# Performance work log

Measured on AMD Instinct MI355X. Metric: run time of the kernel, lower is better.

Reference implementation:

```python
import jax, jax.numpy as jnp
import numpy as np

TAU = 0.5  # matches init_kwargs tau
EPS = 1e-8  # torch CosineSimilarity eps


def setup_inputs() -> dict:
    key = jax.random.key(0)
    k1, k2 = jax.random.split(key)
    B, D = 4096, 256
    return {
        "z_orig": jax.random.normal(k1, (B, D), dtype=jnp.float32),
        "z_augment": jax.random.normal(k2, (B, D), dtype=jnp.float32),
    }


def reference(z_orig, z_augment):
    B = z_orig.shape[0]
    N = 2 * B
    # collect_z = cat([z_augment, z_orig])  -> [2B, D]
    z = jnp.concatenate([z_augment, z_orig], axis=0)
    # cosine similarity matrix via L2 normalize + matmul
    zn = z / jnp.maximum(jnp.linalg.norm(z, axis=-1, keepdims=True), EPS)
    S = zn @ zn.T  # [2B, 2B]
    # positives: diag offsets +B and -B
    pos = jnp.concatenate([jnp.diagonal(S, B), jnp.diagonal(S, -B)])[:, None]  # [2B, 1]
    # negatives: everything except main diag and the +/-B diagonals.
    # Static indices (shape-dependent only), computed in numpy at trace time.
    mask = ~((np.eye(N, k=B) + np.eye(N, k=-B) + np.eye(N)).astype(bool))
    flat_idx = jnp.asarray(np.nonzero(mask.reshape(-1))[0])  # [2B*(2B-2)]
    neg = S.reshape(-1)[flat_idx].reshape(N, N - 2)  # row-major order matches torch boolean mask
    logits = jnp.concatenate([pos, neg], axis=1) / TAU  # [2B, 2B-1]
    # CrossEntropy with label 0 for every row, reduction='sum', then / 2B
    loss = -jax.nn.log_softmax(logits, axis=-1)[:, 0]
    return jnp.sum(loss) / N
```

## Files before the change

kernel.cpp:

```cpp
#include <hip/hip_runtime.h>
#include <hip/hip_bf16.h>

typedef __attribute__((ext_vector_type(8))) short bf16x8;
typedef __attribute__((ext_vector_type(4))) float f32x4;

#define N_ROWS 8192
#define B_HALF 4096
#define D_DIM 256
#define NUT   2080
#define EXP2C 2.885390081777927f

#define WS_ZN       0
#define WS_ROWACC   4194304
#define WS_POS      4227072
#define WS_DIAG     4259840
#define WS_ACC      4292608
#define WS_CNT      4292612

__device__ __forceinline__ unsigned short f2bf(float f) {
    __hip_bfloat16 h = __float2bfloat16(f);
    union { __hip_bfloat16 h; unsigned short u; } c; c.h = h; return c.u;
}

__device__ __forceinline__ float fexp2(float x) { return exp2f(x); }

__device__ __forceinline__ void async_copy16(const void* g, void* l) {
    __builtin_amdgcn_global_load_lds(
        (const __attribute__((address_space(1))) unsigned int*)g,
        (__attribute__((address_space(3))) unsigned int*)l,
        16, 0, 0);
}

__global__ __launch_bounds__(256) void normalize_k(
    const float* __restrict__ z_orig, const float* __restrict__ z_aug,
    unsigned short* __restrict__ zn, float* __restrict__ rowAcc,
    float* __restrict__ accum, unsigned int* __restrict__ cnt)
{
    if (blockIdx.x == 0 && threadIdx.x == 0) { *accum = 0.0f; *cnt = 0u; }
    const int row  = blockIdx.x * 4 + (threadIdx.x >> 6);
    const int lane = threadIdx.x & 63;
    if (lane == 0) rowAcc[row] = 0.0f;
    const float* src = (row < B_HALF) ? (z_aug  + (size_t)row * D_DIM)
                                      : (z_orig + (size_t)(row - B_HALF) * D_DIM);
    float4 v = ((const float4*)src)[lane];
    float ss = v.x*v.x + v.y*v.y + v.z*v.z + v.w*v.w;
    #pragma unroll
    for (int m = 1; m < 64; m <<= 1) ss += __shfl_xor(ss, m);
    float inv = 1.0f / fmaxf(sqrtf(ss), 1e-8f);
    ushort4 o;
    o.x = f2bf(v.x * inv); o.y = f2bf(v.y * inv);
    o.z = f2bf(v.z * inv); o.w = f2bf(v.w * inv);
    ((ushort4*)(zn + (size_t)row * D_DIM))[lane] = o;
}

__global__ __launch_bounds__(256, 3) void tile_k(
    const unsigned short* __restrict__ zn,
    float* __restrict__ rowAcc,
    float* __restrict__ posv,
    float* __restrict__ diagE)
{
    __shared__ unsigned short As[128 * 64];
    __shared__ unsigned short Bs[128 * 64];

    const int bid = blockIdx.x;
    int rb = (int)((129.0f - sqrtf(16641.0f - 8.0f * (float)bid)) * 0.5f);
    rb = rb < 0 ? 0 : (rb > 63 ? 63 : rb);
    while ((rb + 1) * (129 - (rb + 1)) / 2 <= bid) ++rb;
    while (rb * (129 - rb) / 2 > bid) --rb;
    const int cb = rb + (bid - rb * (129 - rb) / 2);

    const int t    = threadIdx.x;
    const int rowBase = rb * 128;
    const int colBase = cb * 128;
    const int lane   = t & 63;
    const int w      = t >> 6;
    const int wy     = w >> 1;
    const int wx     = w & 1;
    const int lane15 = lane & 15;
    const int quad   = lane >> 4;

    f32x4 acc[4][4];
    #pragma unroll
    for (int i = 0; i < 4; ++i)
        #pragma unroll
        for (int j = 0; j < 4; ++j)
            acc[i][j] = (f32x4){0.f, 0.f, 0.f, 0.f};

    const char* zA = (const char*)zn + (size_t)rowBase * 512;
    const char* zB = (const char*)zn + (size_t)colBase * 512;

    const int rloc = t >> 3;
    const int q16  = ((t & 7) ^ (rloc & 7)) * 16;
    const int rA = wy * 64 + lane15;
    const int rB = wx * 64 + lane15;
    const int sw = lane15 & 7;

    #pragma unroll 1
    for (int kk = 0; kk < 4; ++kk) {
        const int koff = kk * 128;
        #pragma unroll
        for (int s = 0; s < 4; ++s) {
            const size_t goff = (size_t)(s * 32 + rloc) * 512 + koff + q16;
            async_copy16(zA + goff, (char*)As + s * 4096 + w * 1024);
            async_copy16(zB + goff, (char*)Bs + s * 4096 + w * 1024);
        }
        __syncthreads();

        #pragma unroll
        for (int kk2 = 0; kk2 < 2; ++kk2) {
            const int pa = (((kk2 * 4 + quad) ^ sw) << 4);
            bf16x8 a[4], b[4];
            #pragma unroll
            for (int mi = 0; mi < 4; ++mi)
                a[mi] = *(const bf16x8*)((const char*)As + (rA + mi * 16) * 128 + pa);
            #pragma unroll
            for (int ni = 0; ni < 4; ++ni)
                b[ni] = *(const bf16x8*)((const char*)Bs + (rB + ni * 16) * 128 + pa);
            #pragma unroll
            for (int mi = 0; mi < 4; ++mi)
                #pragma unroll
                for (int ni = 0; ni < 4; ++ni)
                    acc[mi][ni] = __builtin_amdgcn_mfma_f32_16x16x32_bf16(
                                      a[mi], b[ni], acc[mi][ni], 0, 0, 0);
        }
        __syncthreads();
    }

    const bool diagLane = (wy == wx) && ((lane15 >> 2) == quad);
    const int  rsel = lane15 & 3;
    if (cb == rb && diagLane) {
        #pragma unroll
        for (int mi = 0; mi < 4; ++mi) {
            int grow = rowBase + wy * 64 + mi * 16 + lane15;
            diagE[grow] = fexp2(acc[mi][mi][rsel] * EXP2C);
        }
    }
    if (cb == rb + 32 && diagLane) {
        #pragma unroll
        for (int mi = 0; mi < 4; ++mi) {
            int grow = rowBase + wy * 64 + mi * 16 + lane15;
            float v = acc[mi][mi][rsel];
            posv[grow] = v;
            posv[grow + B_HALF] = v;
        }
    }

    #pragma unroll
    for (int mi = 0; mi < 4; ++mi)
        #pragma unroll
        for (int ni = 0; ni < 4; ++ni)
            #pragma unroll
            for (int r = 0; r < 4; ++r)
                acc[mi][ni][r] = fexp2(acc[mi][ni][r] * EXP2C);

    #pragma unroll
    for (int mi = 0; mi < 4; ++mi)
        #pragma unroll
        for (int r = 0; r < 4; ++r) {
            float s = acc[mi][0][r] + acc[mi][1][r] + acc[mi][2][r] + acc[mi][3][r];
            s += __shfl_xor(s, 1);
            s += __shfl_xor(s, 2);
            s += __shfl_xor(s, 4);
            s += __shfl_xor(s, 8);
            if (lane15 == 0)
                atomicAdd(&rowAcc[rowBase + wy * 64 + mi * 16 + quad * 4 + r], s);
        }

    if (cb != rb) {
        #pragma unroll
        for (int ni = 0; ni < 4; ++ni) {
            float s = 0.0f;
            #pragma unroll
            for (int mi = 0; mi < 4; ++mi)
                s += acc[mi][ni][0] + acc[mi][ni][1] + acc[mi][ni][2] + acc[mi][ni][3];
            s += __shfl_xor(s, 16);
            s += __shfl_xor(s, 32);
            if (quad == 0)
                atomicAdd(&rowAcc[colBase + wx * 64 + ni * 16 + lane15], s);
        }
    }
}

__global__ __launch_bounds__(256) void loss_k(
    const float* __restrict__ rowAcc, const float* __restrict__ posv,
    const float* __restrict__ diagE, float* __restrict__ accum,
    unsigned int* __restrict__ cnt, float* __restrict__ out)
{
    const int i = blockIdx.x * 256 + threadIdx.x;
    float s = rowAcc[i] - diagE[i];
    float loss = __logf(s) - 2.0f * posv[i];

    #pragma unroll
    for (int m = 1; m < 64; m <<= 1) loss += __shfl_xor(loss, m);
    __shared__ float red[4];
    if ((threadIdx.x & 63) == 0) red[threadIdx.x >> 6] = loss;
    __syncthreads();
    if (threadIdx.x == 0) {
        float bs = red[0] + red[1] + red[2] + red[3];
        atomicAdd(accum, bs);
        __threadfence();
        unsigned int old = atomicAdd(cnt, 1u);
        if (old == 31u) {
            __threadfence();
            float total = atomicAdd(accum, 0.0f);
            out[0] = total * (1.0f / (float)N_ROWS);
        }
    }
}

extern "C" void kernel_launch(void* const* d_in, const int* in_sizes, int n_in,
                              void* d_out, int out_size, void* d_ws, size_t ws_size,
                              hipStream_t stream) {
    const float* z_orig = (const float*)d_in[0];
    const float* z_aug  = (const float*)d_in[1];
    char* ws = (char*)d_ws;
    unsigned short* zn  = (unsigned short*)(ws + WS_ZN);
    float* rowAcc       = (float*)(ws + WS_ROWACC);
    float* posv         = (float*)(ws + WS_POS);
    float* diagE        = (float*)(ws + WS_DIAG);
    float* accum        = (float*)(ws + WS_ACC);
    unsigned int* cnt   = (unsigned int*)(ws + WS_CNT);

    normalize_k<<<N_ROWS / 4, 256, 0, stream>>>(z_orig, z_aug, zn, rowAcc, accum, cnt);
    tile_k<<<NUT, 256, 0, stream>>>(zn, rowAcc, posv, diagE);
    loss_k<<<N_ROWS / 256, 256, 0, stream>>>(rowAcc, posv, diagE, accum, cnt,
                                             (float*)d_out);
}
```

Before: 103.7 us.

## Switch similarity GEMM to FP8 MFMA with full-K LDS tiles and row-block reuse

Normalized rows are now stored as FP8 (e4m3) rather than bf16, and the tile kernel uses the fp8 16x16x32 MFMA, which halves operand bytes and doubles MFMA throughput per instruction. Each block keeps its whole 128x256 A row tile resident in LDS and walks up to four column tiles, prefetching the next B tile while the current one's exp/reduction epilogue runs. Grid indexing changes from a triangular bid decode to a 2D grid with early exit. The cost is reduced precision of the cosine similarities, which are then exponentiated, plus 64KB of LDS per block that limits occupancy.

```diff
diff --git a/kernel.cpp b/kernel.cpp
--- a/kernel.cpp
+++ b/kernel.cpp
@@ -1,28 +1,26 @@
 #include <hip/hip_runtime.h>
 #include <hip/hip_bf16.h>
 
-typedef __attribute__((ext_vector_type(8))) short bf16x8;
 typedef __attribute__((ext_vector_type(4))) float f32x4;
 
 #define N_ROWS 8192
 #define B_HALF 4096
-#define D_DIM 256
-#define NUT   2080
 #define EXP2C 2.885390081777927f
 
 #define WS_ZN       0
-#define WS_ROWACC   4194304
-#define WS_POS      4227072
-#define WS_DIAG     4259840
-#define WS_ACC      4292608
-#define WS_CNT      4292612
-
-__device__ __forceinline__ unsigned short f2bf(float f) {
-    __hip_bfloat16 h = __float2bfloat16(f);
-    union { __hip_bfloat16 h; unsigned short u; } c; c.h = h; return c.u;
-}
-
-__device__ __forceinline__ float fexp2(float x) { return exp2f(x); }
+#define WS_ROWACC   2097152
+#define WS_POS      2129920
+#define WS_DIAG     2162688
+#define WS_ACC      2195456
+#define WS_CNT      2195460
+
+__device__ __forceinline__ float fexp2(float x) {
+#if __has_builtin(__builtin_amdgcn_exp2f)
+    return __builtin_amdgcn_exp2f(x);
+#else
+    return exp2f(x);
+#endif
+}
 
 __device__ __forceinline__ void async_copy16(const void* g, void* l) {
     __builtin_amdgcn_global_load_lds(
@@ -33,150 +31,161 @@
 
 __global__ __launch_bounds__(256) void normalize_k(
     const float* __restrict__ z_orig, const float* __restrict__ z_aug,
-    unsigned short* __restrict__ zn, float* __restrict__ rowAcc,
+    unsigned char* __restrict__ zn, float* __restrict__ rowAcc,
     float* __restrict__ accum, unsigned int* __restrict__ cnt)
 {
     if (blockIdx.x == 0 && threadIdx.x == 0) { *accum = 0.0f; *cnt = 0u; }
     const int row  = blockIdx.x * 4 + (threadIdx.x >> 6);
     const int lane = threadIdx.x & 63;
     if (lane == 0) rowAcc[row] = 0.0f;
-    const float* src = (row < B_HALF) ? (z_aug  + (size_t)row * D_DIM)
-                                      : (z_orig + (size_t)(row - B_HALF) * D_DIM);
+    const float* src = (row < B_HALF) ? (z_aug  + (size_t)row * 256)
+                                      : (z_orig + (size_t)(row - B_HALF) * 256);
     float4 v = ((const float4*)src)[lane];
     float ss = v.x*v.x + v.y*v.y + v.z*v.z + v.w*v.w;
     #pragma unroll
     for (int m = 1; m < 64; m <<= 1) ss += __shfl_xor(ss, m);
     float inv = 1.0f / fmaxf(sqrtf(ss), 1e-8f);
-    ushort4 o;
-    o.x = f2bf(v.x * inv); o.y = f2bf(v.y * inv);
-    o.z = f2bf(v.z * inv); o.w = f2bf(v.w * inv);
-    ((ushort4*)(zn + (size_t)row * D_DIM))[lane] = o;
-}
-
-__global__ __launch_bounds__(256, 3) void tile_k(
-    const unsigned short* __restrict__ zn,
+    int pk = 0;
+    pk = __builtin_amdgcn_cvt_pk_fp8_f32(v.x * inv, v.y * inv, pk, false);
+    pk = __builtin_amdgcn_cvt_pk_fp8_f32(v.z * inv, v.w * inv, pk, true);
+    ((int*)(zn + (size_t)row * 256))[lane] = pk;
+}
+
+__global__ __launch_bounds__(256) void tile_k(
+    const unsigned char* __restrict__ zn,
     float* __restrict__ rowAcc,
     float* __restrict__ posv,
     float* __restrict__ diagE)
 {
-    __shared__ unsigned short As[128 * 64];
-    __shared__ unsigned short Bs[128 * 64];
-
-    const int bid = blockIdx.x;
-    int rb = (int)((129.0f - sqrtf(16641.0f - 8.0f * (float)bid)) * 0.5f);
-    rb = rb < 0 ? 0 : (rb > 63 ? 63 : rb);
-    while ((rb + 1) * (129 - (rb + 1)) / 2 <= bid) ++rb;
-    while (rb * (129 - rb) / 2 > bid) --rb;
-    const int cb = rb + (bid - rb * (129 - rb) / 2);
-
-    const int t    = threadIdx.x;
-    const int rowBase = rb * 128;
-    const int colBase = cb * 128;
+    __shared__ unsigned char As[128 * 256];
+    __shared__ unsigned char Bs[128 * 256];
+
+    const int rb  = blockIdx.y;
+    const int cb0 = rb + blockIdx.x * 4;
+    if (cb0 > 63) return;
+    const int nc  = min(4, 64 - cb0);
+
+    const int t      = threadIdx.x;
     const int lane   = t & 63;
     const int w      = t >> 6;
     const int wy     = w >> 1;
     const int wx     = w & 1;
     const int lane15 = lane & 15;
     const int quad   = lane >> 4;
-
-    f32x4 acc[4][4];
+    const int rowBase = rb * 128;
+
+    const int rloc = t >> 4;
+    const int q16  = ((t & 15) ^ rloc) * 16;
+    const int ldsW = w * 1024;
+
+    const unsigned char* gA = zn + (size_t)rowBase * 256;
     #pragma unroll
-    for (int i = 0; i < 4; ++i)
-        #pragma unroll
-        for (int j = 0; j < 4; ++j)
-            acc[i][j] = (f32x4){0.f, 0.f, 0.f, 0.f};
-
-    const char* zA = (const char*)zn + (size_t)rowBase * 512;
-    const char* zB = (const char*)zn + (size_t)colBase * 512;
-
-    const int rloc = t >> 3;
-    const int q16  = ((t & 7) ^ (rloc & 7)) * 16;
-    const int rA = wy * 64 + lane15;
-    const int rB = wx * 64 + lane15;
-    const int sw = lane15 & 7;
-
-    #pragma unroll 1
-    for (int kk = 0; kk < 4; ++kk) {
-        const int koff = kk * 128;
-        #pragma unroll
-        for (int s = 0; s < 4; ++s) {
-            const size_t goff = (size_t)(s * 32 + rloc) * 512 + koff + q16;
-            async_copy16(zA + goff, (char*)As + s * 4096 + w * 1024);
-            async_copy16(zB + goff, (char*)Bs + s * 4096 + w * 1024);
-        }
+    for (int s = 0; s < 8; ++s)
+        async_copy16(gA + (size_t)(s * 16 + rloc) * 256 + q16, As + s * 4096 + ldsW);
+    if (cb0 != rb) {
+        const unsigned char* gB = zn + (size_t)cb0 * 128 * 256;
+        #pragma unroll
+        for (int s = 0; s < 8; ++s)
+            async_copy16(gB + (size_t)(s * 16 + rloc) * 256 + q16, Bs + s * 4096 + ldsW);
+    }
+
+    const int rA = (wy * 64 + lane15) * 256;
+    const int rB = (wx * 64 + lane15) * 256;
+
+    for (int j = 0; j < nc; ++j) {
+        const int cb = cb0 + j;
+        const unsigned char* Bbase = (cb == rb) ? As : Bs;
+
         __syncthreads();
 
-        #pragma unroll
-        for (int kk2 = 0; kk2 < 2; ++kk2) {
-            const int pa = (((kk2 * 4 + quad) ^ sw) << 4);
-            bf16x8 a[4], b[4];
+        f32x4 acc[4][4];
+        #pragma unroll
+        for (int i = 0; i < 4; ++i)
+            #pragma unroll
+            for (int jj = 0; jj < 4; ++jj)
+                acc[i][jj] = (f32x4){0.f, 0.f, 0.f, 0.f};
+
+        #pragma unroll
+        for (int ks = 0; ks < 8; ++ks) {
+            const int sa = (((2 * ks + (quad >> 1)) ^ lane15) << 4) | ((quad & 1) << 3);
+            long a[4], b[4];
             #pragma unroll
             for (int mi = 0; mi < 4; ++mi)
-                a[mi] = *(const bf16x8*)((const char*)As + (rA + mi * 16) * 128 + pa);
+                a[mi] = *(const long*)(As + rA + mi * 4096 + sa);
             #pragma unroll
             for (int ni = 0; ni < 4; ++ni)
-                b[ni] = *(const bf16x8*)((const char*)Bs + (rB + ni * 16) * 128 + pa);
+                b[ni] = *(const long*)(Bbase + rB + ni * 4096 + sa);
             #pragma unroll
             for (int mi = 0; mi < 4; ++mi)
                 #pragma unroll
                 for (int ni = 0; ni < 4; ++ni)
-                    acc[mi][ni] = __builtin_amdgcn_mfma_f32_16x16x32_bf16(
+                    acc[mi][ni] = __builtin_amdgcn_mfma_f32_16x16x32_fp8_fp8(
                                       a[mi], b[ni], acc[mi][ni], 0, 0, 0);
         }
+
         __syncthreads();
-    }
-
-    const bool diagLane = (wy == wx) && ((lane15 >> 2) == quad);
-    const int  rsel = lane15 & 3;
-    if (cb == rb && diagLane) {
-        #pragma unroll
-        for (int mi = 0; mi < 4; ++mi) {
-            int grow = rowBase + wy * 64 + mi * 16 + lane15;
-            diagE[grow] = fexp2(acc[mi][mi][rsel] * EXP2C);
-        }
-    }
-    if (cb == rb + 32 && diagLane) {
-        #pragma unroll
-        for (int mi = 0; mi < 4; ++mi) {
-            int grow = rowBase + wy * 64 + mi * 16 + lane15;
-            float v = acc[mi][mi][rsel];
-            posv[grow] = v;
-            posv[grow + B_HALF] = v;
-        }
-    }
-
-    #pragma unroll
-    for (int mi = 0; mi < 4; ++mi)
-        #pragma unroll
-        for (int ni = 0; ni < 4; ++ni)
-            #pragma unroll
-            for (int r = 0; r < 4; ++r)
-                acc[mi][ni][r] = fexp2(acc[mi][ni][r] * EXP2C);
-
-    #pragma unroll
-    for (int mi = 0; mi < 4; ++mi)
-        #pragma unroll
-        for (int r = 0; r < 4; ++r) {
-            float s = acc[mi][0][r] + acc[mi][1][r] + acc[mi][2][r] + acc[mi][3][r];
-            s += __shfl_xor(s, 1);
-            s += __shfl_xor(s, 2);
-            s += __shfl_xor(s, 4);
-            s += __shfl_xor(s, 8);
-            if (lane15 == 0)
-                atomicAdd(&rowAcc[rowBase + wy * 64 + mi * 16 + quad * 4 + r], s);
-        }
-
-    if (cb != rb) {
-        #pragma unroll
-        for (int ni = 0; ni < 4; ++ni) {
-            float s = 0.0f;
-            #pragma unroll
-            for (int mi = 0; mi < 4; ++mi)
-                s += acc[mi][ni][0] + acc[mi][ni][1] + acc[mi][ni][2] + acc[mi][ni][3];
-            s += __shfl_xor(s, 16);
-            s += __shfl_xor(s, 32);
-            if (quad == 0)
-                atomicAdd(&rowAcc[colBase + wx * 64 + ni * 16 + lane15], s);
+
+        if (j + 1 < nc) {
+            const unsigned char* gB = zn + (size_t)(cb + 1) * 128 * 256;
+            #pragma unroll
+            for (int s = 0; s < 8; ++s)
+                async_copy16(gB + (size_t)(s * 16 + rloc) * 256 + q16,
+                             Bs + s * 4096 + ldsW);
+        }
+
+        const int colBase = cb * 128;
+        const bool diagLane = (wy == wx) && ((lane15 >> 2) == quad);
+        const int  rsel = lane15 & 3;
+        if (cb == rb && diagLane) {
+            #pragma unroll
+            for (int mi = 0; mi < 4; ++mi) {
+                int grow = rowBase + wy * 64 + mi * 16 + lane15;
+                diagE[grow] = fexp2(acc[mi][mi][rsel] * EXP2C);
+            }
+        }
+        if (cb == rb + 32 && diagLane) {
+            #pragma unroll
+            for (int mi = 0; mi < 4; ++mi) {
+                int grow = rowBase + wy * 64 + mi * 16 + lane15;
+                float v = acc[mi][mi][rsel];
+                posv[grow] = v;
+                posv[grow + B_HALF] = v;
+            }
+        }
+
+        #pragma unroll
+        for (int mi = 0; mi < 4; ++mi)
+            #pragma unroll
+            for (int ni = 0; ni < 4; ++ni)
+                #pragma unroll
+                for (int r = 0; r < 4; ++r)
+                    acc[mi][ni][r] = fexp2(acc[mi][ni][r] * EXP2C);
+
+        #pragma unroll
+        for (int mi = 0; mi < 4; ++mi)
+            #pragma unroll
+            for (int r = 0; r < 4; ++r) {
+                float s = acc[mi][0][r] + acc[mi][1][r] + acc[mi][2][r] + acc[mi][3][r];
+                s += __shfl_xor(s, 1);
+                s += __shfl_xor(s, 2);
+                s += __shfl_xor(s, 4);
+                s += __shfl_xor(s, 8);
+                if (lane15 == 0)
+                    atomicAdd(&rowAcc[rowBase + wy * 64 + mi * 16 + quad * 4 + r], s);
+            }
+
+        if (cb != rb) {
+            #pragma unroll
+            for (int ni = 0; ni < 4; ++ni) {
+                float s = 0.0f;
+                #pragma unroll
+                for (int mi = 0; mi < 4; ++mi)
+                    s += acc[mi][ni][0] + acc[mi][ni][1] + acc[mi][ni][2] + acc[mi][ni][3];
+                s += __shfl_xor(s, 16);
+                s += __shfl_xor(s, 32);
+                if (quad == 0)
+                    atomicAdd(&rowAcc[colBase + wx * 64 + ni * 16 + lane15], s);
+            }
         }
     }
 }
@@ -214,7 +223,7 @@
     const float* z_orig = (const float*)d_in[0];
     const float* z_aug  = (const float*)d_in[1];
     char* ws = (char*)d_ws;
-    unsigned short* zn  = (unsigned short*)(ws + WS_ZN);
+    unsigned char* zn   = (unsigned char*)(ws + WS_ZN);
     float* rowAcc       = (float*)(ws + WS_ROWACC);
     float* posv         = (float*)(ws + WS_POS);
     float* diagE        = (float*)(ws + WS_DIAG);
@@ -222,7 +231,7 @@
     unsigned int* cnt   = (unsigned int*)(ws + WS_CNT);
 
     normalize_k<<<N_ROWS / 4, 256, 0, stream>>>(z_orig, z_aug, zn, rowAcc, accum, cnt);
-    tile_k<<<NUT, 256, 0, stream>>>(zn, rowAcc, posv, diagE);
+    tile_k<<<dim3(16, 64), 256, 0, stream>>>(zn, rowAcc, posv, diagE);
     loss_k<<<N_ROWS / 256, 256, 0, stream>>>(rowAcc, posv, diagE, accum, cnt,
                                              (float*)d_out);
 }
```

Measured after the change: 112.1 us. 8.0% more time.
